# Performance work log

Measured on AMD Instinct MI355X. Metric: run time of the kernel, lower is better.

The kernel has to match this reference:

```python
import jax, jax.numpy as jnp
import numpy as np

N_HEADS = 16

def setup_inputs() -> dict:
    key = jax.random.key(0)
    k1, k2, k3, k4 = jax.random.split(key, 4)
    B, N, E = 4, 2048, 1024
    x = jax.random.normal(k1, (B, N, E), dtype=jnp.float32)
    s = 1.0 / np.sqrt(E)
    Wq = jax.random.normal(k2, (E, E), dtype=jnp.float32) * s
    Wk = jax.random.normal(k3, (E, E), dtype=jnp.float32) * s
    Wv = jax.random.normal(k4, (E, E), dtype=jnp.float32) * s
    return {"x": x, "Wq": Wq, "Wk": Wk, "Wv": Wv}

def reference(x, Wq, Wk, Wv):
    # first_block=False -> PositionalEncoding is identity: encoded_vectors = x
    B, N, E = x.shape
    H = N_HEADS
    D = E // H
    norm = np.sqrt(D).astype(np.float32)
    # torch nn.Linear(bias=False): y = x @ W.T
    q = (x @ Wq.T).reshape(B, N, H, D).transpose(0, 2, 1, 3)  # [B,H,N,D]
    k = (x @ Wk.T).reshape(B, N, H, D).transpose(0, 2, 1, 3)
    v = (x @ Wv.T).reshape(B, N, H, D).transpose(0, 2, 1, 3)
    scores = jnp.einsum('bhnd,bhmd->bhnm', q, k) / norm  # [B,H,N,N]
    attn = jax.nn.softmax(scores, axis=-1)
    # original einsum 'stuu, stuv -> stuv': diagonal of attn scales values
    diag = jnp.diagonal(attn, axis1=-2, axis2=-1)  # [B,H,N]
    av = diag[..., None] * v  # [B,H,N,D]
    av = av.transpose(0, 2, 1, 3).reshape(B, N, E)
    return (av, x)
```

## Files before the change

kernel.cpp:

```cpp
#include <hip/hip_runtime.h>
#include <hip/hip_bf16.h>
#include <stdint.h>

typedef __attribute__((ext_vector_type(8))) short short8;
typedef __attribute__((ext_vector_type(4))) float f32x4;

#define BATCH 4
#define SEQ   2048
#define EMB   1024
#define HEADS 16
#define DHEAD 64
#define MROWS (BATCH * SEQ)

#define QSCALE 0.18033688011112042f

__device__ inline unsigned short f2bf(float f) {
    unsigned int u = __float_as_uint(f);
    unsigned int r = (u + 0x7fffu + ((u >> 16) & 1u)) >> 16;
    return (unsigned short)r;
}

__device__ __forceinline__ void gl_lds16(const short* g, short* l) {
    __builtin_amdgcn_global_load_lds(
        (const __attribute__((address_space(1))) void*)g,
        (__attribute__((address_space(3))) void*)l, 16, 0, 0);
}

__global__ __launch_bounds__(256) void pack_x(const float* __restrict__ src,
                                              unsigned short* __restrict__ dst,
                                              float* __restrict__ pass) {
    int i = (blockIdx.x * 256 + threadIdx.x) * 8;
    const float4* s = reinterpret_cast<const float4*>(src + i);
    float4 f0 = s[0];
    float4 f1 = s[1];
    union { unsigned short u[8]; short8 v; } o;
    o.u[0] = f2bf(f0.x); o.u[1] = f2bf(f0.y); o.u[2] = f2bf(f0.z); o.u[3] = f2bf(f0.w);
    o.u[4] = f2bf(f1.x); o.u[5] = f2bf(f1.y); o.u[6] = f2bf(f1.z); o.u[7] = f2bf(f1.w);
    *reinterpret_cast<short8*>(dst + i) = o.v;
    float4* p = reinterpret_cast<float4*>(pass + i);
    p[0] = f0;
    p[1] = f1;
}

__global__ __launch_bounds__(256) void pack_w3(const float* __restrict__ wq,
                                               const float* __restrict__ wk,
                                               const float* __restrict__ wv,
                                               unsigned short* __restrict__ dq,
                                               unsigned short* __restrict__ dk,
                                               unsigned short* __restrict__ dv) {
    const float* src = blockIdx.y == 0 ? wq : blockIdx.y == 1 ? wk : wv;
    unsigned short* dst = blockIdx.y == 0 ? dq : blockIdx.y == 1 ? dk : dv;
    int i = (blockIdx.x * 256 + threadIdx.x) * 8;
    const float4* s = reinterpret_cast<const float4*>(src + i);
    float4 f0 = s[0];
    float4 f1 = s[1];
    union { unsigned short u[8]; short8 v; } o;
    o.u[0] = f2bf(f0.x); o.u[1] = f2bf(f0.y); o.u[2] = f2bf(f0.z); o.u[3] = f2bf(f0.w);
    o.u[4] = f2bf(f1.x); o.u[5] = f2bf(f1.y); o.u[6] = f2bf(f1.z); o.u[7] = f2bf(f1.w);
    *reinterpret_cast<short8*>(dst + i) = o.v;
}

template <int MODE>
__global__ __launch_bounds__(256) void gemm_bt(const short* __restrict__ A,
                                               const short* __restrict__ Bm,
                                               unsigned short* __restrict__ Cb,
                                               float* __restrict__ out,
                                               const float* __restrict__ dgp) {
    constexpr int K = EMB;
    __shared__ short As[128 * 32];
    __shared__ short Bs[128 * 32];
    const int m0 = blockIdx.x * 128;
    const int n0 = blockIdx.y * 128;
    const int t = threadIdx.x;
    const int lane = t & 63;
    const int w = t >> 6;
    const int wr = w >> 1, wc = w & 1;

    f32x4 acc[4][4] = {};

    const short* gA = A + (size_t)(m0 + (t >> 2)) * K + (t & 3) * 8;
    const short* gB = Bm + (size_t)(n0 + (t >> 2)) * K + (t & 3) * 8;
    short* lA0 = As + w * 512;
    short* lA1 = As + 2048 + w * 512;
    short* lB0 = Bs + w * 512;
    short* lB1 = Bs + 2048 + w * 512;

    const int kq = (lane >> 4) * 8;
    const int fr = lane & 15;

    for (int k0 = 0; k0 < K; k0 += 32) {
        gl_lds16(gA + k0, lA0);
        gl_lds16(gA + 64 * K + k0, lA1);
        gl_lds16(gB + k0, lB0);
        gl_lds16(gB + 64 * K + k0, lB1);
        __syncthreads();

        short8 a[4], b[4];
#pragma unroll
        for (int i = 0; i < 4; i++)
            a[i] = *(const short8*)&As[(wr * 64 + i * 16 + fr) * 32 + kq];
#pragma unroll
        for (int j = 0; j < 4; j++)
            b[j] = *(const short8*)&Bs[(wc * 64 + j * 16 + fr) * 32 + kq];
#pragma unroll
        for (int i = 0; i < 4; i++)
#pragma unroll
            for (int j = 0; j < 4; j++)
                acc[i][j] = __builtin_amdgcn_mfma_f32_16x16x32_bf16(a[i], b[j], acc[i][j], 0, 0, 0);
        __syncthreads();
    }

    const int gr_base = m0 + wr * 64 + (lane >> 4) * 4;
    const int gc_base = n0 + wc * 64 + fr;
#pragma unroll
    for (int i = 0; i < 4; i++) {
#pragma unroll
        for (int j = 0; j < 4; j++) {
            const int col = gc_base + j * 16;
#pragma unroll
            for (int r = 0; r < 4; r++) {
                const int grow = gr_base + i * 16 + r;
                const int bb = grow >> 11;
                const int nn = grow & 2047;
                if (MODE == 0) {
                    const int sel = col >> 10;
                    const int cc = col & 1023;
                    const int hh = cc >> 6;
                    const int dd = cc & 63;
                    const float sc = sel ? 1.0f : QSCALE;
                    Cb[(((size_t)((sel << 6) + (bb << 4) + hh) * SEQ + nn) << 6) + dd] =
                        f2bf(acc[i][j][r] * sc);
                } else {
                    const int hh = col >> 6;
                    const float d = dgp[((bb << 4) + hh) * SEQ + nn];
                    out[(size_t)grow * EMB + col] = acc[i][j][r] * d;
                }
            }
        }
    }
}

#define KT 128

__global__ __launch_bounds__(512, 4) void diag_kernel(const short* __restrict__ Qh,
                                                      const short* __restrict__ Kh,
                                                      float* __restrict__ dgp) {
    const int n = blockIdx.x;
    const int bh = (n & 7) | ((n >> 6) << 3);
    const int qt = (n >> 3) & 7;
    __shared__ short Ks[2][KT][64];

    const int t = threadIdx.x;
    const int lane = t & 63;
    const int w = t >> 6;
    const int rl = lane & 15;
    const int g = lane >> 4;
    const int kq = g * 8;

    const short* Kbh = Kh + (size_t)bh * SEQ * DHEAD;
    const short* Qbh = Qh + (size_t)bh * SEQ * DHEAD;

    const int qbase = qt * 256 + w * 32;
    short8 a0[2], a1[2];
#pragma unroll
    for (int i = 0; i < 2; i++) {
        const int qrow = qbase + i * 16 + rl;
        a0[i] = *(const short8*)(Qbh + qrow * DHEAD + kq);
        a1[i] = *(const short8*)(Qbh + qrow * DHEAD + kq + 32);
    }

    float sdiag[2];
    const int rr = rl - g * 4;
#pragma unroll
    for (int i = 0; i < 2; i++) {
        const int krow = qbase + i * 16 + rl;
        const short8 b0d = *(const short8*)(Kbh + krow * DHEAD + kq);
        const short8 b1d = *(const short8*)(Kbh + krow * DHEAD + kq + 32);
        f32x4 cd = {};
        cd = __builtin_amdgcn_mfma_f32_16x16x32_bf16(a0[i], b0d, cd, 0, 0, 0);
        cd = __builtin_amdgcn_mfma_f32_16x16x32_bf16(a1[i], b1d, cd, 0, 0, 0);
        sdiag[i] = (rr >= 0 && rr < 4) ? cd[rr] : 0.f;
    }

    const int r0 = t >> 3;
    const int c0 = t & 7;
    const int cs = (c0 ^ (r0 & 7)) * 8;

    *(short8*)&Ks[0][r0][cs]      = *(const short8*)&Kbh[r0 * DHEAD + c0 * 8];
    *(short8*)&Ks[0][r0 + 64][cs] = *(const short8*)&Kbh[(r0 + 64) * DHEAD + c0 * 8];
    __syncthreads();

    const int blk0 = (g ^ (lane & 7)) * 8;
    const int blk1 = ((g + 4) ^ (lane & 7)) * 8;

    float ssum[2][4] = {};
    int buf = 0;

    for (int kt = 0; kt < SEQ / KT; ++kt) {
        short8 p0, p1;
        if (kt < SEQ / KT - 1) {
            const short* src = Kbh + (kt + 1) * KT * DHEAD;
            p0 = *(const short8*)&src[r0 * DHEAD + c0 * 8];
            p1 = *(const short8*)&src[(r0 + 64) * DHEAD + c0 * 8];
        }
#pragma unroll
        for (int sub = 0; sub < 8; ++sub) {
            const int row = sub * 16 + rl;
            const short8 b0 = *(const short8*)&Ks[buf][row][blk0];
            const short8 b1 = *(const short8*)&Ks[buf][row][blk1];
            f32x4 c[2];
#pragma unroll
            for (int i = 0; i < 2; i++) {
                c[i] = __builtin_amdgcn_mfma_f32_16x16x32_bf16(a0[i], b0, f32x4{}, 0, 0, 0);
                c[i] = __builtin_amdgcn_mfma_f32_16x16x32_bf16(a1[i], b1, c[i], 0, 0, 0);
            }
#pragma unroll
            for (int i = 0; i < 2; i++)
#pragma unroll
                for (int r = 0; r < 4; ++r)
                    ssum[i][r] += __builtin_amdgcn_exp2f(c[i][r]);
        }
        if (kt < SEQ / KT - 1) {
            __syncthreads();
            *(short8*)&Ks[buf ^ 1][r0][cs]      = p0;
            *(short8*)&Ks[buf ^ 1][r0 + 64][cs] = p1;
            __syncthreads();
        }
        buf ^= 1;
    }

#pragma unroll
    for (int i = 0; i < 2; i++)
#pragma unroll
        for (int r = 0; r < 4; r++) {
            float v = ssum[i][r];
            v += __shfl_xor(v, 1);
            v += __shfl_xor(v, 2);
            v += __shfl_xor(v, 4);
            v += __shfl_xor(v, 8);
            ssum[i][r] = v;
        }

    if (rr >= 0 && rr < 4) {
#pragma unroll
        for (int i = 0; i < 2; i++) {
            const float dg = __builtin_amdgcn_exp2f(sdiag[i]) / ssum[i][rr];
            dgp[bh * SEQ + qbase + i * 16 + rl] = dg;
        }
    }
}

extern "C" void kernel_launch(void* const* d_in, const int* in_sizes, int n_in,
                              void* d_out, int out_size, void* d_ws, size_t ws_size,
                              hipStream_t stream) {
    const float* x  = (const float*)d_in[0];
    const float* Wq = (const float*)d_in[1];
    const float* Wk = (const float*)d_in[2];
    const float* Wv = (const float*)d_in[3];
    float* out = (float*)d_out;
    char* ws = (char*)d_ws;

    const size_t xb_off  = 0;
    const size_t wq_off  = xb_off + (size_t)MROWS * EMB * 2;
    const size_t wk_off  = wq_off + (size_t)EMB * EMB * 2;
    const size_t wv_off  = wk_off + (size_t)EMB * EMB * 2;
    const size_t q_off   = wv_off + (size_t)EMB * EMB * 2;
    const size_t k_off   = q_off + (size_t)MROWS * EMB * 2;
    const size_t dg_off  = k_off + (size_t)MROWS * EMB * 2;

    short* xb  = (short*)(ws + xb_off);
    short* wqb = (short*)(ws + wq_off);
    short* wkb = (short*)(ws + wk_off);
    short* wvb = (short*)(ws + wv_off);
    short* Qh  = (short*)(ws + q_off);
    short* Kh  = (short*)(ws + k_off);
    float* dgp = (float*)(ws + dg_off);

    const int nx = MROWS * EMB;
    const int nw = EMB * EMB;

    pack_x<<<nx / 2048, 256, 0, stream>>>(x, (unsigned short*)xb,
                                          out + (size_t)MROWS * EMB);
    pack_w3<<<dim3(nw / 2048, 3), 256, 0, stream>>>(Wq, Wk, Wv,
                                                    (unsigned short*)wqb,
                                                    (unsigned short*)wkb,
                                                    (unsigned short*)wvb);

    gemm_bt<0><<<dim3(MROWS / 128, 2048 / 128), 256, 0, stream>>>(
        xb, wqb, (unsigned short*)Qh, nullptr, nullptr);

    diag_kernel<<<BATCH * HEADS * (SEQ / 256), 512, 0, stream>>>(Qh, Kh, dgp);

    gemm_bt<1><<<dim3(MROWS / 128, EMB / 128), 256, 0, stream>>>(
        xb, wvb, nullptr, out, dgp);
}
```

Before: 138.8 us.

## Rewrite projection GEMMs with larger tiles and triple-buffered async LDS pipeline

Replaces the 128x128, 256-thread GEMM with a 512-thread kernel using 256x256 (QK) or 256x128 (V) tiles. Global loads go straight into LDS through a three-stage ring with prefetch two k-steps ahead, synchronised by explicit vmcnt waits and one barrier per step instead of two. It also adds an XOR swizzle on LDS fragments and raises wave priority around the MFMA block. The aim is to hide memory latency and raise data reuse per tile, at the cost of more LDS and more registers per block, which may lower occupancy.

Result: faster. 129.3 us (-6.9%).

```diff
diff --git a/kernel.cpp b/kernel.cpp
--- a/kernel.cpp
+++ b/kernel.cpp
@@ -24,6 +24,11 @@
     __builtin_amdgcn_global_load_lds(
         (const __attribute__((address_space(1))) void*)g,
         (__attribute__((address_space(3))) void*)l, 16, 0, 0);
+}
+
+template <int N>
+__device__ __forceinline__ void waitvm() {
+    asm volatile("s_waitcnt vmcnt(%0)" :: "n"(N) : "memory");
 }
 
 __global__ __launch_bounds__(256) void pack_x(const float* __restrict__ src,
@@ -61,61 +66,99 @@
 }
 
 template <int MODE>
-__global__ __launch_bounds__(256) void gemm_bt(const short* __restrict__ A,
-                                               const short* __restrict__ Bm,
-                                               unsigned short* __restrict__ Cb,
-                                               float* __restrict__ out,
-                                               const float* __restrict__ dgp) {
+__global__ __launch_bounds__(512, 2) void gemm8(const short* __restrict__ A,
+                                                const short* __restrict__ Bm,
+                                                unsigned short* __restrict__ Cb,
+                                                float* __restrict__ out,
+                                                const float* __restrict__ dgp) {
     constexpr int K = EMB;
-    __shared__ short As[128 * 32];
-    __shared__ short Bs[128 * 32];
-    const int m0 = blockIdx.x * 128;
-    const int n0 = blockIdx.y * 128;
+    constexpr int NT = K / 32;
+    constexpr int BN = (MODE == 0) ? 256 : 128;
+    constexpr int NF = BN / 64;
+    constexpr int BUFSTRIDE = 8192 + BN * 32;
+    constexpr int VW = 2 + BN / 128;
+
+    __shared__ short Ks[3 * BUFSTRIDE];
+
     const int t = threadIdx.x;
     const int lane = t & 63;
     const int w = t >> 6;
-    const int wr = w >> 1, wc = w & 1;
-
-    f32x4 acc[4][4] = {};
-
-    const short* gA = A + (size_t)(m0 + (t >> 2)) * K + (t & 3) * 8;
-    const short* gB = Bm + (size_t)(n0 + (t >> 2)) * K + (t & 3) * 8;
-    short* lA0 = As + w * 512;
-    short* lA1 = As + 2048 + w * 512;
-    short* lB0 = Bs + w * 512;
-    short* lB1 = Bs + 2048 + w * 512;
-
-    const int kq = (lane >> 4) * 8;
-    const int fr = lane & 15;
-
-    for (int k0 = 0; k0 < K; k0 += 32) {
-        gl_lds16(gA + k0, lA0);
-        gl_lds16(gA + 64 * K + k0, lA1);
-        gl_lds16(gB + k0, lB0);
-        gl_lds16(gB + 64 * K + k0, lB1);
-        __syncthreads();
-
-        short8 a[4], b[4];
-#pragma unroll
-        for (int i = 0; i < 4; i++)
-            a[i] = *(const short8*)&As[(wr * 64 + i * 16 + fr) * 32 + kq];
-#pragma unroll
-        for (int j = 0; j < 4; j++)
-            b[j] = *(const short8*)&Bs[(wc * 64 + j * 16 + fr) * 32 + kq];
-#pragma unroll
-        for (int i = 0; i < 4; i++)
-#pragma unroll
-            for (int j = 0; j < 4; j++)
-                acc[i][j] = __builtin_amdgcn_mfma_f32_16x16x32_bf16(a[i], b[j], acc[i][j], 0, 0, 0);
-        __syncthreads();
-    }
-
-    const int gr_base = m0 + wr * 64 + (lane >> 4) * 4;
-    const int gc_base = n0 + wc * 64 + fr;
-#pragma unroll
-    for (int i = 0; i < 4; i++) {
-#pragma unroll
-        for (int j = 0; j < 4; j++) {
+    const int wr = w >> 2;
+    const int wc = w & 3;
+    const int rl = lane & 15;
+    const int pg = (lane >> 4) ^ (lane & 3);
+    const int m0 = blockIdx.x * 256;
+    const int n0 = blockIdx.y * BN;
+
+    const int sr = t >> 2;
+    const int sg = (t & 3) ^ (sr & 3);
+    const int soff = sr * K + sg * 8;
+    const short* gA0 = A + (size_t)(m0)*K + soff;
+    const short* gA1 = A + (size_t)(m0 + 128) * K + soff;
+    const short* gB0 = Bm + (size_t)(n0)*K + soff;
+    const short* gB1 = Bm + (size_t)(n0 + 128) * K + soff;
+    short* ldsw = Ks + w * 512;
+
+#define STAGE8(kk, bb)                                               \
+    {                                                                \
+        const int _k = (kk)*32;                                      \
+        short* _l = ldsw + (bb)*BUFSTRIDE;                           \
+        gl_lds16(gA0 + _k, _l);                                      \
+        gl_lds16(gA1 + _k, _l + 4096);                               \
+        gl_lds16(gB0 + _k, _l + 8192);                               \
+        if (MODE == 0) gl_lds16(gB1 + _k, _l + 12288);               \
+    }
+
+    f32x4 acc[8][NF] = {};
+
+    STAGE8(0, 0);
+    STAGE8(1, 1);
+    waitvm<VW>();
+    __builtin_amdgcn_s_barrier();
+
+    int cur = 0;
+    for (int kt = 0; kt < NT; ++kt) {
+        const int pf = kt + 2;
+        if (pf < NT) {
+            int nb = cur + 2; if (nb >= 3) nb -= 3;
+            STAGE8(pf, nb);
+        }
+
+        const short* bufp = Ks + cur * BUFSTRIDE;
+        short8 av[8], bv[NF];
+#pragma unroll
+        for (int i = 0; i < 8; i++)
+            av[i] = *(const short8*)&bufp[wr * 4096 + i * 512 + rl * 32 + pg * 8];
+#pragma unroll
+        for (int j = 0; j < NF; j++) {
+            const int brow = (MODE == 0) ? ((wc & 1) * 64 + j * 16 + rl)
+                                         : (wc * 32 + j * 16 + rl);
+            const int bh = (MODE == 0) ? (wc >> 1) : 0;
+            bv[j] = *(const short8*)&bufp[8192 + bh * 4096 + brow * 32 + pg * 8];
+        }
+
+        __builtin_amdgcn_s_setprio(1);
+#pragma unroll
+        for (int i = 0; i < 8; i++)
+#pragma unroll
+            for (int j = 0; j < NF; j++)
+                acc[i][j] = __builtin_amdgcn_mfma_f32_16x16x32_bf16(av[i], bv[j], acc[i][j], 0, 0, 0);
+        __builtin_amdgcn_s_setprio(0);
+
+        if (kt < NT - 2) waitvm<VW>();
+        else             waitvm<0>();
+        __builtin_amdgcn_s_barrier();
+
+        cur += 1; if (cur == 3) cur = 0;
+    }
+#undef STAGE8
+
+    const int gr_base = m0 + wr * 128 + (lane >> 4) * 4;
+    const int gc_base = n0 + wc * (BN / 4) + rl;
+#pragma unroll
+    for (int i = 0; i < 8; i++) {
+#pragma unroll
+        for (int j = 0; j < NF; j++) {
             const int col = gc_base + j * 16;
 #pragma unroll
             for (int r = 0; r < 4; r++) {
@@ -148,7 +191,7 @@
     const int n = blockIdx.x;
     const int bh = (n & 7) | ((n >> 6) << 3);
     const int qt = (n >> 3) & 7;
-    __shared__ short Ks[2][KT][64];
+    __shared__ short Ksd[2][KT][64];
 
     const int t = threadIdx.x;
     const int lane = t & 63;
@@ -186,8 +229,8 @@
     const int c0 = t & 7;
     const int cs = (c0 ^ (r0 & 7)) * 8;
 
-    *(short8*)&Ks[0][r0][cs]      = *(const short8*)&Kbh[r0 * DHEAD + c0 * 8];
-    *(short8*)&Ks[0][r0 + 64][cs] = *(const short8*)&Kbh[(r0 + 64) * DHEAD + c0 * 8];
+    *(short8*)&Ksd[0][r0][cs]      = *(const short8*)&Kbh[r0 * DHEAD + c0 * 8];
+    *(short8*)&Ksd[0][r0 + 64][cs] = *(const short8*)&Kbh[(r0 + 64) * DHEAD + c0 * 8];
     __syncthreads();
 
     const int blk0 = (g ^ (lane & 7)) * 8;
@@ -206,8 +249,8 @@
 #pragma unroll
         for (int sub = 0; sub < 8; ++sub) {
             const int row = sub * 16 + rl;
-            const short8 b0 = *(const short8*)&Ks[buf][row][blk0];
-            const short8 b1 = *(const short8*)&Ks[buf][row][blk1];
+            const short8 b0 = *(const short8*)&Ksd[buf][row][blk0];
+            const short8 b1 = *(const short8*)&Ksd[buf][row][blk1];
             f32x4 c[2];
 #pragma unroll
             for (int i = 0; i < 2; i++) {
@@ -222,8 +265,8 @@
         }
         if (kt < SEQ / KT - 1) {
             __syncthreads();
-            *(short8*)&Ks[buf ^ 1][r0][cs]      = p0;
-            *(short8*)&Ks[buf ^ 1][r0 + 64][cs] = p1;
+            *(short8*)&Ksd[buf ^ 1][r0][cs]      = p0;
+            *(short8*)&Ksd[buf ^ 1][r0 + 64][cs] = p1;
             __syncthreads();
         }
         buf ^= 1;
@@ -286,11 +329,11 @@
                                                     (unsigned short*)wkb,
                                                     (unsigned short*)wvb);
 
-    gemm_bt<0><<<dim3(MROWS / 128, 2048 / 128), 256, 0, stream>>>(
+    gemm8<0><<<dim3(MROWS / 256, 2048 / 256), 512, 0, stream>>>(
         xb, wqb, (unsigned short*)Qh, nullptr, nullptr);
 
     diag_kernel<<<BATCH * HEADS * (SEQ / 256), 512, 0, stream>>>(Qh, Kh, dgp);
 
-    gemm_bt<1><<<dim3(MROWS / 128, EMB / 128), 256, 0, stream>>>(
+    gemm8<1><<<dim3(MROWS / 256, EMB / 128), 512, 0, stream>>>(
         xb, wvb, nullptr, out, dgp);
 }
```
